# Kernel optimization log

Measured on AMD Instinct MI355X. Metric: run time of the kernel, lower is better.

Reference implementation:

```python
import jax, jax.numpy as jnp
import numpy as np
from jax import lax


def quick_gelu(x):
    return x * jax.nn.sigmoid(1.702 * x)


def setup_inputs() -> dict:
    key = jax.random.key(0)
    ks = jax.random.split(key, 12)
    B, H, W, C, D, M = 32, 56, 56, 192, 64, 8
    g = lambda k, shape, s: (jax.random.normal(k, shape, jnp.float32) * s)
    return {
        "x": jax.random.normal(ks[0], (B, H, W, C), jnp.float32),
        "W1": g(ks[1], (64, C), 0.05),
        "b1": jnp.zeros((64,), jnp.float32),
        "W2": g(ks[2], (64, 64), 0.05),
        "b2": jnp.zeros((64,), jnp.float32),
        "mask_token": g(ks[3], (M, 64), 0.05),
        "Wh": g(ks[4], (D * D * 9, 64), 0.02),
        "bh": g(ks[5], (D * D * 9,), 0.02),
        "Wd": g(ks[6], (D, C), 0.05),
        "bd": jnp.zeros((D,), jnp.float32),
        "Wu": g(ks[7], (C, D), 0.02),
        "bu": jnp.zeros((C,), jnp.float32),
    }


def reference(x, W1, b1, W2, b2, mask_token, Wh, bh, Wd, bd, Wu, bu):
    B, H, W_, C = x.shape
    D = Wd.shape[0]
    M = mask_token.shape[0]
    # meta_net: Linear -> ReLU -> Linear, [B,H,W,64]
    pf = jax.nn.relu(jnp.einsum("bhwc,kc->bhwk", x, W1) + b1)
    pf = jnp.einsum("bhwk,jk->bhwj", pf, W2) + b2
    # mask routing: [M,B,H,W], softmax over spatial positions
    mask = jnp.einsum("bhwk,mk->mbhw", pf, mask_token)
    mask = jax.nn.softmax(mask.reshape(M, B, -1), axis=-1).reshape(M, B, H, W_)
    # sum_m mask[m][...,None]*pf, then sum over H,W -> [B,64]
    mwf = (mask.sum(0)[..., None] * pf).sum(axis=(1, 2))
    # hypernet: per-sample conv weights [B,D,D,3,3]
    conv_w = (jnp.einsum("bk,ok->bo", mwf, Wh) + bh).reshape(B, D, D, 3, 3)
    # adapter_down + QuickGELU, [B,D,H,W]
    xd = jnp.einsum("bhwc,dc->bhwd", x, Wd) + bd
    xp = quick_gelu(xd.transpose(0, 3, 1, 2))

    def conv1(xi, wi):  # xi [D,H,W], wi [D,D,3,3]
        return lax.conv_general_dilated(xi[None], wi, (1, 1), [(1, 1), (1, 1)])[0]

    xc = jax.vmap(conv1)(xp, conv_w)  # [B,D,H,W]
    xd2 = quick_gelu(xc.transpose(0, 2, 3, 1))  # [B,H,W,D]
    # dropout(p=0.1) is identity in eval mode
    xu = jnp.einsum("bhwd,cd->bhwc", xd2, Wu) + bu
    return xu + x
```

## Files before the change

kernel.cpp:

```cpp
#include <hip/hip_runtime.h>

typedef unsigned short ushort_t;
typedef short bf16x8 __attribute__((ext_vector_type(8)));
typedef float f32x4 __attribute__((ext_vector_type(4)));

#define MFMA(a, b, c) __builtin_amdgcn_mfma_f32_16x16x32_bf16(a, b, c, 0, 0, 0)

#define B_    32
#define HW_   3136
#define NPOS  100352

__device__ __forceinline__ float bf2f(unsigned short h) {
    return __uint_as_float(((unsigned int)h) << 16);
}
__device__ __forceinline__ unsigned short f2bf(float f) {
    unsigned int u = __float_as_uint(f);
    u += 0x7FFFu + ((u >> 16) & 1u);
    return (unsigned short)(u >> 16);
}
__device__ __forceinline__ float qgelu(float v) {
    return v / (1.0f + __expf(-1.702f * v));
}
__device__ __forceinline__ void unpack8(uint4 v, float* f) {
    f[0] = bf2f((unsigned short)(v.x & 0xffff)); f[1] = bf2f((unsigned short)(v.x >> 16));
    f[2] = bf2f((unsigned short)(v.y & 0xffff)); f[3] = bf2f((unsigned short)(v.y >> 16));
    f[4] = bf2f((unsigned short)(v.z & 0xffff)); f[5] = bf2f((unsigned short)(v.z >> 16));
    f[6] = bf2f((unsigned short)(v.w & 0xffff)); f[7] = bf2f((unsigned short)(v.w >> 16));
}

__global__ __launch_bounds__(256) void k0_prep(
    const float* __restrict__ W1, const float* __restrict__ W2,
    const float* __restrict__ mtok, const float* __restrict__ Wd,
    const float* __restrict__ Wu,
    ushort_t* __restrict__ w1f, ushort_t* __restrict__ wdf,
    ushort_t* __restrict__ w2f, ushort_t* __restrict__ mtf,
    ushort_t* __restrict__ wuf)
{
    const int gid = blockIdx.x * 256 + threadIdx.x;
    const int stride = gridDim.x * 256;
    for (int i = gid; i < 12288; i += stride) {
        int j = i & 7, lane = (i >> 3) & 63, nt = (i >> 9) & 3, kc = i >> 11;
        int n = nt * 16 + (lane & 15), k = kc * 32 + (lane >> 4) * 8 + j;
        w1f[i] = f2bf(W1[n * 192 + k]);
        wdf[i] = f2bf(Wd[n * 192 + k]);
    }
    for (int i = gid; i < 4096; i += stride) {
        int j = i & 7, lane = (i >> 3) & 63, nt = (i >> 9) & 3, kc = i >> 11;
        int n = nt * 16 + (lane & 15), k = kc * 32 + (lane >> 4) * 8 + j;
        w2f[i] = f2bf(W2[n * 64 + k]);
    }
    for (int i = gid; i < 1024; i += stride) {
        int j = i & 7, lane = (i >> 3) & 63, kc = i >> 9;
        int n = lane & 15, k = kc * 32 + (lane >> 4) * 8 + j;
        mtf[i] = (n < 8) ? f2bf(mtok[n * 64 + k]) : (ushort_t)0;
    }
    for (int i = gid; i < 12288; i += stride) {
        int j = i & 7, lane = (i >> 3) & 63, g = i >> 9;
        int nt = g % 12, kc = g / 12;
        int n = nt * 16 + (lane & 15), k = kc * 32 + (lane >> 4) * 8 + j;
        wuf[i] = f2bf(Wu[n * 64 + k]);
    }
}

__global__ __launch_bounds__(256, 2) void k1_meta_adapter(
    const float* __restrict__ x, const float* __restrict__ b1,
    const float* __restrict__ b2, const float* __restrict__ bd,
    const ushort_t* __restrict__ w1f, const ushort_t* __restrict__ wdf,
    const ushort_t* __restrict__ w2f, const ushort_t* __restrict__ mtf,
    ushort_t* __restrict__ pf2g, ushort_t* __restrict__ xpg,
    float* __restrict__ Lg)
{
    __shared__ ushort_t pf1s[64 * 72];
    __shared__ ushort_t pf2s[64 * 72];
    __shared__ ushort_t xps[64 * 72];

    const int tid = threadIdx.x;
    const int lane = tid & 63, wv = tid >> 6;
    const int col = lane & 15, q = lane >> 4;
    const int posBase = blockIdx.x * 64;

    bf16x8 B1r[6], Bdr[6], B2r[2], Bmr[2];
    #pragma unroll
    for (int kc = 0; kc < 6; kc++) {
        B1r[kc] = *(const bf16x8*)(w1f + ((kc * 4 + wv) * 64 + lane) * 8);
        Bdr[kc] = *(const bf16x8*)(wdf + ((kc * 4 + wv) * 64 + lane) * 8);
    }
    #pragma unroll
    for (int kc = 0; kc < 2; kc++) {
        B2r[kc] = *(const bf16x8*)(w2f + ((kc * 4 + wv) * 64 + lane) * 8);
        Bmr[kc] = *(const bf16x8*)(mtf + (kc * 64 + lane) * 8);
    }

    const float bias1 = b1[wv * 16 + col];
    const float biasd = bd[wv * 16 + col];
    const float bias2 = b2[wv * 16 + col];

    f32x4 acc1[4], acc3[4];
    #pragma unroll
    for (int m = 0; m < 4; m++) { acc1[m] = (f32x4)0.0f; acc3[m] = (f32x4)0.0f; }

    #pragma unroll
    for (int kc = 0; kc < 6; kc++) {
        bf16x8 A[4];
        #pragma unroll
        for (int m = 0; m < 4; m++) {
            const float4* gp = (const float4*)(x +
                (size_t)(posBase + m * 16 + col) * 192 + kc * 32 + q * 8);
            float4 v0 = gp[0], v1 = gp[1];
            A[m][0] = (short)f2bf(v0.x); A[m][1] = (short)f2bf(v0.y);
            A[m][2] = (short)f2bf(v0.z); A[m][3] = (short)f2bf(v0.w);
            A[m][4] = (short)f2bf(v1.x); A[m][5] = (short)f2bf(v1.y);
            A[m][6] = (short)f2bf(v1.z); A[m][7] = (short)f2bf(v1.w);
        }
        #pragma unroll
        for (int m = 0; m < 4; m++) {
            acc1[m] = MFMA(A[m], B1r[kc], acc1[m]);
            acc3[m] = MFMA(A[m], Bdr[kc], acc3[m]);
        }
    }

    #pragma unroll
    for (int m = 0; m < 4; m++)
        #pragma unroll
        for (int r = 0; r < 4; r++)
            pf1s[(m * 16 + q * 4 + r) * 72 + wv * 16 + col] =
                f2bf(fmaxf(acc1[m][r] + bias1, 0.0f));
    __syncthreads();

    f32x4 acc2[4];
    #pragma unroll
    for (int m = 0; m < 4; m++) acc2[m] = (f32x4)0.0f;
    #pragma unroll
    for (int kc = 0; kc < 2; kc++) {
        #pragma unroll
        for (int m = 0; m < 4; m++) {
            bf16x8 A2 = *(const bf16x8*)&pf1s[(m * 16 + col) * 72 + kc * 32 + q * 8];
            acc2[m] = MFMA(A2, B2r[kc], acc2[m]);
        }
    }

    #pragma unroll
    for (int m = 0; m < 4; m++)
        #pragma unroll
        for (int r = 0; r < 4; r++) {
            xps[(m * 16 + q * 4 + r) * 72 + wv * 16 + col] =
                f2bf(qgelu(acc3[m][r] + biasd));
            pf2s[(m * 16 + q * 4 + r) * 72 + wv * 16 + col] =
                f2bf(acc2[m][r] + bias2);
        }
    __syncthreads();

    f32x4 Lacc = (f32x4)0.0f;
    #pragma unroll
    for (int kc = 0; kc < 2; kc++) {
        bf16x8 A3 = *(const bf16x8*)&pf2s[(wv * 16 + col) * 72 + kc * 32 + q * 8];
        Lacc = MFMA(A3, Bmr[kc], Lacc);
    }
    if (col < 8) {
        #pragma unroll
        for (int r = 0; r < 4; r++)
            Lg[((size_t)(posBase + wv * 16 + q * 4 + r)) * 8 + col] = Lacc[r];
    }

    #pragma unroll
    for (int t = 0; t < 2; t++) {
        int u = tid + t * 256;
        int pos = u >> 3, c8 = u & 7;
        uint4 vx = *(const uint4*)&xps[pos * 72 + c8 * 8];
        *(uint4*)(xpg + ((size_t)(posBase + pos)) * 64 + c8 * 8) = vx;
        uint4 vp = *(const uint4*)&pf2s[pos * 72 + c8 * 8];
        *(uint4*)(pf2g + ((size_t)(posBase + pos)) * 64 + c8 * 8) = vp;
    }
}

__global__ __launch_bounds__(256) void k2a_partial(
    const float* __restrict__ Lg, float* __restrict__ Pmax, float* __restrict__ Psum,
    float* __restrict__ mwfg)
{
    __shared__ float wred[4][8];
    __shared__ float Msh[8];

    const int tid = threadIdx.x;
    const int b = blockIdx.x >> 3, sl = blockIdx.x & 7;
    const int lane = tid & 63, wv = tid >> 6;
    const float* Lb = Lg + ((size_t)b * HW_ + (size_t)sl * 392) * 8;

    if (blockIdx.x == 0)
        for (int i = tid; i < 2048; i += 256) mwfg[i] = 0.0f;

    float l0[8], l1[8];
    {
        const float4* p = (const float4*)(Lb + (size_t)tid * 8);
        float4 a = p[0], c = p[1];
        l0[0] = a.x; l0[1] = a.y; l0[2] = a.z; l0[3] = a.w;
        l0[4] = c.x; l0[5] = c.y; l0[6] = c.z; l0[7] = c.w;
    }
    if (tid < 136) {
        const float4* p = (const float4*)(Lb + (size_t)(tid + 256) * 8);
        float4 a = p[0], c = p[1];
        l1[0] = a.x; l1[1] = a.y; l1[2] = a.z; l1[3] = a.w;
        l1[4] = c.x; l1[5] = c.y; l1[6] = c.z; l1[7] = c.w;
    } else {
        #pragma unroll
        for (int m = 0; m < 8; m++) l1[m] = -1e30f;
    }

    float lm[8];
    #pragma unroll
    for (int m = 0; m < 8; m++) {
        float v = fmaxf(l0[m], l1[m]);
        for (int off = 32; off > 0; off >>= 1) v = fmaxf(v, __shfl_down(v, off));
        lm[m] = v;
    }
    if (lane == 0) {
        #pragma unroll
        for (int m = 0; m < 8; m++) wred[wv][m] = lm[m];
    }
    __syncthreads();
    if (tid < 8)
        Msh[tid] = fmaxf(fmaxf(wred[0][tid], wred[1][tid]), fmaxf(wred[2][tid], wred[3][tid]));
    __syncthreads();

    float s[8];
    #pragma unroll
    for (int m = 0; m < 8; m++)
        s[m] = __expf(l0[m] - Msh[m]) + __expf(l1[m] - Msh[m]);
    #pragma unroll
    for (int m = 0; m < 8; m++) {
        float v = s[m];
        for (int off = 32; off > 0; off >>= 1) v += __shfl_down(v, off);
        s[m] = v;
    }
    __syncthreads();
    if (lane == 0) {
        #pragma unroll
        for (int m = 0; m < 8; m++) wred[wv][m] = s[m];
    }
    __syncthreads();
    if (tid < 8) {
        Psum[((size_t)b * 8 + sl) * 8 + tid] =
            wred[0][tid] + wred[1][tid] + wred[2][tid] + wred[3][tid];
        Pmax[((size_t)b * 8 + sl) * 8 + tid] = Msh[tid];
    }
}

__global__ __launch_bounds__(256) void k2c_mwf(
    const float* __restrict__ Lg, const ushort_t* __restrict__ pf2g,
    const float* __restrict__ Pmax, const float* __restrict__ Psum,
    float* __restrict__ mwfg)
{
    __shared__ float ms[392];
    __shared__ float sred[32 * 64];

    const int tid = threadIdx.x;
    const int b = blockIdx.x >> 3, sl = blockIdx.x & 7;
    const size_t base = (size_t)b * HW_ + (size_t)sl * 392;

    float smx[8], sinv[8];
    #pragma unroll
    for (int m = 0; m < 8; m++) {
        float M = -1e30f;
        #pragma unroll
        for (int s2 = 0; s2 < 8; s2++)
            M = fmaxf(M, Pmax[((size_t)b * 8 + s2) * 8 + m]);
        float S = 0.0f;
        #pragma unroll
        for (int s2 = 0; s2 < 8; s2++)
            S += Psum[((size_t)b * 8 + s2) * 8 + m] *
                 __expf(Pmax[((size_t)b * 8 + s2) * 8 + m] - M);
        smx[m] = M; sinv[m] = 1.0f / S;
    }

    for (int lp = tid; lp < 392; lp += 256) {
        const float4* p = (const float4*)(Lg + (base + lp) * 8);
        float4 a = p[0], c = p[1];
        ms[lp] = __expf(a.x - smx[0]) * sinv[0] + __expf(a.y - smx[1]) * sinv[1]
               + __expf(a.z - smx[2]) * sinv[2] + __expf(a.w - smx[3]) * sinv[3]
               + __expf(c.x - smx[4]) * sinv[4] + __expf(c.y - smx[5]) * sinv[5]
               + __expf(c.z - smx[6]) * sinv[6] + __expf(c.w - smx[7]) * sinv[7];
    }
    __syncthreads();

    const int part = tid >> 3, kg = tid & 7;
    float a8[8];
    #pragma unroll
    for (int j = 0; j < 8; j++) a8[j] = 0.0f;
    for (int lp = part; lp < 392; lp += 32) {
        float w = ms[lp];
        uint4 v = *(const uint4*)(pf2g + (base + lp) * 64 + kg * 8);
        float f[8]; unpack8(v, f);
        #pragma unroll
        for (int j = 0; j < 8; j++) a8[j] += w * f[j];
    }
    #pragma unroll
    for (int j = 0; j < 8; j++) sred[part * 64 + kg * 8 + j] = a8[j];
    __syncthreads();
    if (tid < 64) {
        float s = 0.0f;
        #pragma unroll
        for (int pt = 0; pt < 32; pt++) s += sred[pt * 64 + tid];
        atomicAdd(&mwfg[b * 64 + tid], s);
    }
}

__global__ __launch_bounds__(256) void k3_hypernet(
    const float* __restrict__ mwfg, const float* __restrict__ Whg,
    const float* __restrict__ bhg, ushort_t* __restrict__ cwb)
{
    __shared__ float mwfs[32 * 64];
    const int tid = threadIdx.x;
    for (int i = tid; i < 2048; i += 256) mwfs[i] = mwfg[i];
    __syncthreads();

    const int op = blockIdx.x * 64 + (tid >> 2);
    const int bq = tid & 3;
    const int j = op & 7, lane = (op >> 3) & 63, nt = (op >> 9) & 3;
    const int kc = (op >> 11) & 1, tap = op >> 12;
    const int oc = nt * 16 + (lane & 15);
    const int ic = kc * 32 + (lane >> 4) * 8 + j;
    const int o = oc * 576 + ic * 9 + tap;

    float wreg[64];
    const float4* src = (const float4*)(Whg + (size_t)o * 64);
    #pragma unroll
    for (int t = 0; t < 16; t++) {
        float4 v = src[t];
        wreg[t * 4 + 0] = v.x; wreg[t * 4 + 1] = v.y;
        wreg[t * 4 + 2] = v.z; wreg[t * 4 + 3] = v.w;
    }
    const float bias = bhg[o];
    #pragma unroll
    for (int i = 0; i < 8; i += 2) {
        int b0 = bq * 8 + i, b1 = b0 + 1;
        float a0 = bias, a1 = bias;
        #pragma unroll
        for (int k = 0; k < 64; k++) {
            a0 += mwfs[b0 * 64 + k] * wreg[k];
            a1 += mwfs[b1 * 64 + k] * wreg[k];
        }
        cwb[(size_t)b0 * 36864 + op] = f2bf(a0);
        cwb[(size_t)b1 * 36864 + op] = f2bf(a1);
    }
}

__global__ __launch_bounds__(256, 4) void k4_conv(
    const ushort_t* __restrict__ xpg, const ushort_t* __restrict__ cwb,
    ushort_t* __restrict__ xd2g)
{
    __shared__ ushort_t xs[2 * 232 * 40];

    const int tid = threadIdx.x;
    const int bid = blockIdx.x;
    const int swz = (bid & 7) * 112 + (bid >> 3);
    const int b = swz / 28, yt = swz % 28, y0 = yt * 2;

    for (int u = tid; u < 1856; u += 256) {
        int r = u / 464, rem = u % 464, c = rem >> 3, c8 = rem & 7;
        int gy = y0 - 1 + r, gx = c - 1;
        uint4 v = make_uint4(0, 0, 0, 0);
        if (gy >= 0 && gy < 56 && gx >= 0 && gx < 56)
            v = *(const uint4*)(xpg + ((size_t)b * HW_ + gy * 56 + gx) * 64 + c8 * 8);
        int kc = c8 >> 2, q = c8 & 3;
        *(uint4*)&xs[kc * 9280 + (r * 58 + c) * 40 + q * 8] = v;
    }
    __syncthreads();

    const int lane = tid & 63, wv = tid >> 6;
    const int col = lane & 15, q = lane >> 4;

    int abase[7];
    #pragma unroll
    for (int t = 0; t < 7; t++) {
        int p = t * 16 + col;
        int row = p / 56, cc = p - row * 56;
        abase[t] = ((row * 58 + cc) * 40 + q * 8) * 2;
    }

    f32x4 acc[7];
    #pragma unroll
    for (int t = 0; t < 7; t++) acc[t] = (f32x4)0.0f;

    const ushort_t* wbase = cwb + (size_t)b * 36864;
    #pragma unroll
    for (int tap = 0; tap < 9; tap++) {
        const int dy = tap / 3, dx = tap % 3;
        const int toff = (dy * 58 + dx) * 80;
        bf16x8 Bf0 = *(const bf16x8*)(wbase + tap * 4096 + ((0 * 4 + wv) * 64 + lane) * 8);
        bf16x8 Bf1 = *(const bf16x8*)(wbase + tap * 4096 + ((1 * 4 + wv) * 64 + lane) * 8);
        #pragma unroll
        for (int t = 0; t < 7; t++) {
            bf16x8 A0 = *(const bf16x8*)((const char*)xs + abase[t] + toff);
            bf16x8 A1 = *(const bf16x8*)((const char*)xs + 18560 + abase[t] + toff);
            acc[t] = MFMA(A0, Bf0, acc[t]);
            acc[t] = MFMA(A1, Bf1, acc[t]);
        }
    }
    __syncthreads();

    #pragma unroll
    for (int t = 0; t < 7; t++)
        #pragma unroll
        for (int r = 0; r < 4; r++)
            xs[(t * 16 + q * 4 + r) * 72 + wv * 16 + col] = f2bf(qgelu(acc[t][r]));
    __syncthreads();

    for (int u = tid; u < 896; u += 256) {
        int pos = u >> 3, c8 = u & 7;
        uint4 v = *(const uint4*)&xs[pos * 72 + c8 * 8];
        size_t gpos = (size_t)b * HW_ + (size_t)y0 * 56 + pos;
        *(uint4*)(xd2g + gpos * 64 + c8 * 8) = v;
    }
}

__global__ __launch_bounds__(256, 2) void k5_up_res(
    const ushort_t* __restrict__ xd2g, const ushort_t* __restrict__ wuf,
    const float* __restrict__ bu, const float* __restrict__ xg,
    float* __restrict__ outg)
{
    const int tid = threadIdx.x;
    const int lane = tid & 63, wv = tid >> 6;
    const int col = lane & 15, q = lane >> 4;
    const size_t posBase = (size_t)blockIdx.x * 64;

    bf16x8 Bw[2][3];
    #pragma unroll
    for (int kc = 0; kc < 2; kc++)
        #pragma unroll
        for (int nt = 0; nt < 3; nt++)
            Bw[kc][nt] = *(const bf16x8*)(wuf + ((kc * 12 + wv * 3 + nt) * 64 + lane) * 8);

    bf16x8 A[4][2];
    #pragma unroll
    for (int m = 0; m < 4; m++)
        #pragma unroll
        for (int kc = 0; kc < 2; kc++)
            A[m][kc] = *(const bf16x8*)(xd2g +
                (posBase + m * 16 + col) * 64 + kc * 32 + q * 8);

    float biasu[3];
    #pragma unroll
    for (int nt = 0; nt < 3; nt++) biasu[nt] = bu[(wv * 3 + nt) * 16 + col];

    f32x4 acc[4][3];
    #pragma unroll
    for (int m = 0; m < 4; m++)
        #pragma unroll
        for (int nt = 0; nt < 3; nt++) acc[m][nt] = (f32x4)0.0f;

    #pragma unroll
    for (int kc = 0; kc < 2; kc++)
        #pragma unroll
        for (int m = 0; m < 4; m++)
            #pragma unroll
            for (int nt = 0; nt < 3; nt++)
                acc[m][nt] = MFMA(A[m][kc], Bw[kc][nt], acc[m][nt]);

    #pragma unroll
    for (int m = 0; m < 4; m++)
        #pragma unroll
        for (int nt = 0; nt < 3; nt++)
            #pragma unroll
            for (int r = 0; r < 4; r++) {
                size_t off = (posBase + m * 16 + q * 4 + r) * 192 + (wv * 3 + nt) * 16 + col;
                outg[off] = acc[m][nt][r] + biasu[nt] + xg[off];
            }
}

extern "C" void kernel_launch(void* const* d_in, const int* in_sizes, int n_in,
                              void* d_out, int out_size, void* d_ws, size_t ws_size,
                              hipStream_t stream) {
    const float* x    = (const float*)d_in[0];
    const float* W1   = (const float*)d_in[1];
    const float* b1   = (const float*)d_in[2];
    const float* W2   = (const float*)d_in[3];
    const float* b2   = (const float*)d_in[4];
    const float* mtok = (const float*)d_in[5];
    const float* Wh   = (const float*)d_in[6];
    const float* bh   = (const float*)d_in[7];
    const float* Wd   = (const float*)d_in[8];
    const float* bd   = (const float*)d_in[9];
    const float* Wu   = (const float*)d_in[10];
    const float* bu   = (const float*)d_in[11];
    float* out = (float*)d_out;

    char* ws = (char*)d_ws;
    ushort_t* pf2 = (ushort_t*)ws;
    ushort_t* xp  = (ushort_t*)(ws + 12845056);
    ushort_t* xd2 = pf2;
    ushort_t* cwb = (ushort_t*)(ws + 25690112);
    float*    mwf = (float*)(ws + 28049408);
    float*    Lg  = (float*)(ws + 28057600);
    ushort_t* w1f = (ushort_t*)(ws + 31268864);
    ushort_t* wdf = (ushort_t*)(ws + 31293440);
    ushort_t* w2f = (ushort_t*)(ws + 31318016);
    ushort_t* mtf = (ushort_t*)(ws + 31326208);
    ushort_t* wuf = (ushort_t*)(ws + 31328256);
    float*    Pmax= (float*)(ws + 31352832);
    float*    Psum= (float*)(ws + 31361024);

    k0_prep<<<48, 256, 0, stream>>>(W1, W2, mtok, Wd, Wu, w1f, wdf, w2f, mtf, wuf);
    k1_meta_adapter<<<1568, 256, 0, stream>>>(x, b1, b2, bd, w1f, wdf, w2f, mtf,
                                              pf2, xp, Lg);
    k2a_partial<<<256, 256, 0, stream>>>(Lg, Pmax, Psum, mwf);
    k2c_mwf<<<256, 256, 0, stream>>>(Lg, pf2, Pmax, Psum, mwf);
    k3_hypernet<<<576, 256, 0, stream>>>(mwf, Wh, bh, cwb);
    k4_conv<<<896, 256, 0, stream>>>(xp, cwb, xd2);
    k5_up_res<<<1568, 256, 0, stream>>>(xd2, wuf, bu, x, out);
}
```

Before: 256.4 us.

## Double-buffer x loads in meta kernel and stage up-projection operands through LDS

In k1 the per-chunk global loads of x are now software-pipelined: the next K chunk is loaded into a second register buffer while the current one is converted and fed to MFMA, with a sched_barrier after the weight preload and the min-blocks hint removed from launch bounds. In k5 the Wu fragments and the 64-position xd2 tile are copied into shared memory, and each wave now covers 16 rows across all 12 output tiles instead of 4 row tiles by 3 column tiles. The occupancy hint is raised to 4 blocks. This is meant to hide global load latency and raise occupancy, at the cost of extra LDS traffic, a block-wide sync, and possibly more register pressure in k1 without its occupancy hint.

```diff
diff --git a/kernel.cpp b/kernel.cpp
--- a/kernel.cpp
+++ b/kernel.cpp
@@ -62,7 +62,7 @@
     }
 }
 
-__global__ __launch_bounds__(256, 2) void k1_meta_adapter(
+__global__ __launch_bounds__(256) void k1_meta_adapter(
     const float* __restrict__ x, const float* __restrict__ b1,
     const float* __restrict__ b2, const float* __restrict__ bd,
     const ushort_t* __restrict__ w1f, const ushort_t* __restrict__ wdf,
@@ -90,6 +90,7 @@
         B2r[kc] = *(const bf16x8*)(w2f + ((kc * 4 + wv) * 64 + lane) * 8);
         Bmr[kc] = *(const bf16x8*)(mtf + (kc * 64 + lane) * 8);
     }
+    __builtin_amdgcn_sched_barrier(0);
 
     const float bias1 = b1[wv * 16 + col];
     const float biasd = bd[wv * 16 + col];
@@ -99,23 +100,44 @@
     #pragma unroll
     for (int m = 0; m < 4; m++) { acc1[m] = (f32x4)0.0f; acc3[m] = (f32x4)0.0f; }
 
+    float4 xv0[4][2], xv1[4][2];
+    #pragma unroll
+    for (int m = 0; m < 4; m++) {
+        const float4* gp = (const float4*)(x +
+            (size_t)(posBase + m * 16 + col) * 192 + 0 * 32 + q * 8);
+        xv0[m][0] = gp[0]; xv0[m][1] = gp[1];
+    }
+
     #pragma unroll
     for (int kc = 0; kc < 6; kc++) {
-        bf16x8 A[4];
+        if (kc < 5) {
+            if ((kc & 1) == 0) {
+                #pragma unroll
+                for (int m = 0; m < 4; m++) {
+                    const float4* gp = (const float4*)(x +
+                        (size_t)(posBase + m * 16 + col) * 192 + (kc + 1) * 32 + q * 8);
+                    xv1[m][0] = gp[0]; xv1[m][1] = gp[1];
+                }
+            } else {
+                #pragma unroll
+                for (int m = 0; m < 4; m++) {
+                    const float4* gp = (const float4*)(x +
+                        (size_t)(posBase + m * 16 + col) * 192 + (kc + 1) * 32 + q * 8);
+                    xv0[m][0] = gp[0]; xv0[m][1] = gp[1];
+                }
+            }
+        }
         #pragma unroll
         for (int m = 0; m < 4; m++) {
-            const float4* gp = (const float4*)(x +
-                (size_t)(posBase + m * 16 + col) * 192 + kc * 32 + q * 8);
-            float4 v0 = gp[0], v1 = gp[1];
-            A[m][0] = (short)f2bf(v0.x); A[m][1] = (short)f2bf(v0.y);
-            A[m][2] = (short)f2bf(v0.z); A[m][3] = (short)f2bf(v0.w);
-            A[m][4] = (short)f2bf(v1.x); A[m][5] = (short)f2bf(v1.y);
-            A[m][6] = (short)f2bf(v1.z); A[m][7] = (short)f2bf(v1.w);
-        }
-        #pragma unroll
-        for (int m = 0; m < 4; m++) {
-            acc1[m] = MFMA(A[m], B1r[kc], acc1[m]);
-            acc3[m] = MFMA(A[m], Bdr[kc], acc3[m]);
+            float4 v0 = ((kc & 1) == 0) ? xv0[m][0] : xv1[m][0];
+            float4 v1 = ((kc & 1) == 0) ? xv0[m][1] : xv1[m][1];
+            bf16x8 A;
+            A[0] = (short)f2bf(v0.x); A[1] = (short)f2bf(v0.y);
+            A[2] = (short)f2bf(v0.z); A[3] = (short)f2bf(v0.w);
+            A[4] = (short)f2bf(v1.x); A[5] = (short)f2bf(v1.y);
+            A[6] = (short)f2bf(v1.z); A[7] = (short)f2bf(v1.w);
+            acc1[m] = MFMA(A, B1r[kc], acc1[m]);
+            acc3[m] = MFMA(A, Bdr[kc], acc3[m]);
         }
     }
 
@@ -412,58 +434,59 @@
     }
 }
 
-__global__ __launch_bounds__(256, 2) void k5_up_res(
+__global__ __launch_bounds__(256, 4) void k5_up_res(
     const ushort_t* __restrict__ xd2g, const ushort_t* __restrict__ wuf,
     const float* __restrict__ bu, const float* __restrict__ xg,
     float* __restrict__ outg)
 {
+    __shared__ ushort_t xds[64 * 72];
+    __shared__ ushort_t wsh[12288];
+
     const int tid = threadIdx.x;
+    const size_t posBase = (size_t)blockIdx.x * 64;
+
+    {
+        uint4* d = (uint4*)wsh;
+        const uint4* s = (const uint4*)wuf;
+        for (int u = tid; u < 1536; u += 256) d[u] = s[u];
+    }
+    #pragma unroll
+    for (int t = 0; t < 2; t++) {
+        int u = tid + t * 256;
+        int pos = u >> 3, c8 = u & 7;
+        uint4 v = *(const uint4*)(xd2g + (posBase + pos) * 64 + c8 * 8);
+        *(uint4*)&xds[pos * 72 + c8 * 8] = v;
+    }
+    __syncthreads();
+
     const int lane = tid & 63, wv = tid >> 6;
     const int col = lane & 15, q = lane >> 4;
-    const size_t posBase = (size_t)blockIdx.x * 64;
-
-    bf16x8 Bw[2][3];
+
+    bf16x8 A[2];
     #pragma unroll
     for (int kc = 0; kc < 2; kc++)
-        #pragma unroll
-        for (int nt = 0; nt < 3; nt++)
-            Bw[kc][nt] = *(const bf16x8*)(wuf + ((kc * 12 + wv * 3 + nt) * 64 + lane) * 8);
-
-    bf16x8 A[4][2];
-    #pragma unroll
-    for (int m = 0; m < 4; m++)
-        #pragma unroll
-        for (int kc = 0; kc < 2; kc++)
-            A[m][kc] = *(const bf16x8*)(xd2g +
-                (posBase + m * 16 + col) * 64 + kc * 32 + q * 8);
-
-    float biasu[3];
-    #pragma unroll
-    for (int nt = 0; nt < 3; nt++) biasu[nt] = bu[(wv * 3 + nt) * 16 + col];
-
-    f32x4 acc[4][3];
-    #pragma unroll
-    for (int m = 0; m < 4; m++)
-        #pragma unroll
-        for (int nt = 0; nt < 3; nt++) acc[m][nt] = (f32x4)0.0f;
-
+        A[kc] = *(const bf16x8*)&xds[(wv * 16 + col) * 72 + kc * 32 + q * 8];
+
+    f32x4 acc[12];
+    #pragma unroll
+    for (int nt = 0; nt < 12; nt++) acc[nt] = (f32x4)0.0f;
     #pragma unroll
     for (int kc = 0; kc < 2; kc++)
         #pragma unroll
-        for (int m = 0; m < 4; m++)
-            #pragma unroll
-            for (int nt = 0; nt < 3; nt++)
-                acc[m][nt] = MFMA(A[m][kc], Bw[kc][nt], acc[m][nt]);
-
-    #pragma unroll
-    for (int m = 0; m < 4; m++)
-        #pragma unroll
-        for (int nt = 0; nt < 3; nt++)
-            #pragma unroll
-            for (int r = 0; r < 4; r++) {
-                size_t off = (posBase + m * 16 + q * 4 + r) * 192 + (wv * 3 + nt) * 16 + col;
-                outg[off] = acc[m][nt][r] + biasu[nt] + xg[off];
-            }
+        for (int nt = 0; nt < 12; nt++) {
+            bf16x8 B = *(const bf16x8*)&wsh[((kc * 12 + nt) * 64 + lane) * 8];
+            acc[nt] = MFMA(A[kc], B, acc[nt]);
+        }
+
+    #pragma unroll
+    for (int nt = 0; nt < 12; nt++) {
+        float bias = bu[nt * 16 + col];
+        #pragma unroll
+        for (int r = 0; r < 4; r++) {
+            size_t off = (posBase + wv * 16 + q * 4 + r) * 192 + nt * 16 + col;
+            outg[off] = acc[nt][r] + bias + xg[off];
+        }
+    }
 }
 
 extern "C" void kernel_launch(void* const* d_in, const int* in_sizes, int n_in,
```

After: 250.2 us. -2.4%, faster.
